# Kernel tuning notes

Hardware: AMD Instinct MI355X
Metric: run time of the kernel (lower is better)

The kernel has to match this reference:

```python
import jax, jax.numpy as jnp
import numpy as np

N, E, G = 50000, 600000, 512   # nodes, edges, graphs
F, D, L = 128, 128, 3          # in_features, hidden dim, num_gc_layers
ED = D * L                      # embedding_dim (readout='concat')
C = 1.0                         # curvature
MIN_NORM = 1e-15
BALL_EPS = 4e-3                 # hgcn PoincareBall proj eps for float32


def _logmap0(p, c):
    sc = jnp.sqrt(c)
    n = jnp.clip(jnp.linalg.norm(p, axis=-1, keepdims=True), MIN_NORM, None)
    return p / (sc * n) * jnp.arctanh(jnp.clip(sc * n, -1 + 1e-15, 1 - 1e-15))


def _expmap0(u, c):
    sc = jnp.sqrt(c)
    n = jnp.clip(jnp.linalg.norm(u, axis=-1, keepdims=True), MIN_NORM, None)
    return jnp.tanh(sc * n) * u / (sc * n)


def _proj(x, c):
    n = jnp.clip(jnp.linalg.norm(x, axis=-1, keepdims=True), MIN_NORM, None)
    maxn = (1.0 - BALL_EPS) / jnp.sqrt(c)
    return jnp.where(n > maxn, x / n * maxn, x)


def _gcn(x, W, b, src, dst):
    h = x @ W
    deg = jax.ops.segment_sum(jnp.ones_like(dst, dtype=h.dtype), dst, num_segments=N) + 1.0
    dinv = deg ** -0.5
    msg = h[src] * (dinv[src] * dinv[dst])[:, None]           # [E, D]
    agg = jax.ops.segment_sum(msg, dst, num_segments=N) + h * (dinv * dinv)[:, None]
    return agg + b


def _encoder(x, Ws, bs, src, dst, batch):
    xs = []
    for W, b in zip(Ws, bs):
        x = jax.nn.relu(_gcn(x, W, b, src, dst))
        xs.append(x)
    # readout='concat' with global_add_pool
    g = jnp.concatenate([jax.ops.segment_sum(h, batch, num_segments=G) for h in xs], axis=1)
    return g, jnp.concatenate(xs, axis=1)


def _mlp(x, W1, W2):  # proj_head: Linear (no bias), ReLU, Linear (no bias)
    return jax.nn.relu(x @ W1) @ W2


def setup_inputs() -> dict:
    key = jax.random.key(0)
    ks = jax.random.split(key, 24)

    def xav(k, i, o):
        return jax.random.normal(k, (i, o), dtype=jnp.float32) * np.float32(np.sqrt(2.0 / (i + o)))

    inp = {
        'x':   jax.random.normal(ks[0], (N, F), dtype=jnp.float32) * 1e-3,  # points inside the ball
        'x_s': jax.random.normal(ks[1], (N, F), dtype=jnp.float32) * 1e-3,
        'src': jax.random.randint(ks[2], (E,), 0, N, dtype=jnp.int32),
        'dst': jax.random.randint(ks[3], (E,), 0, N, dtype=jnp.int32),
        'batch': jnp.sort(jax.random.randint(ks[4], (N,), 0, G, dtype=jnp.int32)),
        # feature-branch GCN encoder
        'Wf0': xav(ks[5], F, D), 'Wf1': xav(ks[6], D, D), 'Wf2': xav(ks[7], D, D),
        'bf0': jnp.zeros((D,), jnp.float32), 'bf1': jnp.zeros((D,), jnp.float32), 'bf2': jnp.zeros((D,), jnp.float32),
        # structure-branch GCN encoder
        'Ws0': xav(ks[8], F, D), 'Ws1': xav(ks[9], D, D), 'Ws2': xav(ks[10], D, D),
        'bs0': jnp.zeros((D,), jnp.float32), 'bs1': jnp.zeros((D,), jnp.float32), 'bs2': jnp.zeros((D,), jnp.float32),
        # proj heads (biases removed by init_emb)
        'P1': xav(ks[11], ED, ED), 'P2': xav(ks[12], ED, ED),
        'G1': xav(ks[13], 2 * ED, ED), 'G2': xav(ks[14], ED, ED),
    }
    return inp


def reference(x, x_s, Wf0, Wf1, Wf2, bf0, bf1, bf2, Ws0, Ws1, Ws2, bs0, bs1, bs2, P1, P2, G1, G2, src, dst, batch):
    xt_f = _logmap0(x, C)
    xt_s = _logmap0(x_s, C)
    g_f, n_f = _encoder(xt_f, (Wf0, Wf1, Wf2), (bf0, bf1, bf2), src, dst, batch)
    g_s, n_s = _encoder(xt_s, (Ws0, Ws1, Ws2), (bs0, bs1, bs2), src, dst, batch)
    g = _mlp(jnp.concatenate((g_f, g_s), axis=1), G1, G2)
    e = lambda t: _proj(_expmap0(t, C), C)
    return (e(g), e(_mlp(g_f, P1, P2)), e(_mlp(n_f, P1, P2)), e(_mlp(g_s, P1, P2)), e(_mlp(n_s, P1, P2)))
```

## Files before the change

### kernel.cpp

```cpp
#include <hip/hip_runtime.h>
#include <math.h>

#define N_NODES 50000
#define N_EDGES 600000
#define N_GRAPHS 512
#define F_IN 128
#define D_HID 128
#define EDIM 384
#define M_ALL (N_NODES + N_GRAPHS)

typedef __attribute__((ext_vector_type(8))) short bf16x8;
typedef __attribute__((ext_vector_type(4))) float f32x4;
typedef __attribute__((ext_vector_type(16))) float f32x16;

static __device__ __forceinline__ float wave_reduce_sum(float s) {
#pragma unroll
  for (int off = 32; off > 0; off >>= 1) s += __shfl_xor(s, off, 64);
  return s;
}

static __device__ __forceinline__ int wave_reduce_sum_i(int s) {
#pragma unroll
  for (int off = 32; off > 0; off >>= 1) s += __shfl_xor(s, off, 64);
  return s;
}

static __device__ __forceinline__ short f2b(float f) {
  unsigned u = __float_as_uint(f);
  unsigned r = (u + 0x7FFFu + ((u >> 16) & 1u)) >> 16;
  return (short)r;
}

static __device__ __forceinline__ float b2f(short s) {
  return __uint_as_float(((unsigned)(unsigned short)s) << 16);
}


#define SCAN_BS 256
#define SCAN_NB ((N_NODES + SCAN_BS - 1) / SCAN_BS)

__global__ __launch_bounds__(SCAN_BS) void init_kernel(const int* __restrict__ batch,
                                                       int* __restrict__ cnt,
                                                       int* __restrict__ gptr) {
  int i = blockIdx.x * SCAN_BS + threadIdx.x;
  if (i < N_NODES) cnt[i] = 0;
  if (i <= N_GRAPHS) {
    int lo = 0, hi = N_NODES;
    while (lo < hi) { int mid = (lo + hi) >> 1; if (batch[mid] < i) lo = mid + 1; else hi = mid; }
    gptr[i] = lo;
  }
}

__global__ void hist_kernel(const int* __restrict__ dst, int* __restrict__ cnt) {
  int i = blockIdx.x * blockDim.x + threadIdx.x;
  if (i < N_EDGES) atomicAdd(&cnt[dst[i]], 1);
}

__global__ __launch_bounds__(SCAN_BS) void scan1_kernel(const int* __restrict__ cnt,
                                                        int* __restrict__ row_ptr,
                                                        int* __restrict__ bsum) {
  __shared__ int wsum[4];
  int tid = threadIdx.x, lane = tid & 63, wid = tid >> 6;
  int idx = blockIdx.x * SCAN_BS + tid;
  int v = (idx < N_NODES) ? cnt[idx] : 0;
  int x = v;
#pragma unroll
  for (int off = 1; off < 64; off <<= 1) {
    int t = __shfl_up(x, off, 64);
    if (lane >= off) x += t;
  }
  if (lane == 63) wsum[wid] = x;
  __syncthreads();
  int pre = 0, tot = 0;
#pragma unroll
  for (int w = 0; w < 4; ++w) { int s = wsum[w]; tot += s; if (w < wid) pre += s; }
  if (idx < N_NODES) row_ptr[idx + 1] = x + pre;
  if (tid == 0) bsum[blockIdx.x] = tot;
}

__global__ __launch_bounds__(SCAN_BS) void scan3_kernel(const int* __restrict__ cnt,
                                                        const int* __restrict__ bsum,
                                                        int* __restrict__ row_ptr,
                                                        int* __restrict__ cursor,
                                                        float* __restrict__ dinv) {
  __shared__ int ws[4];
  int tid = threadIdx.x, lane = tid & 63, wid = tid >> 6;
  int v = 0;
  if (tid < SCAN_NB && tid < blockIdx.x) v = bsum[tid];
  v = wave_reduce_sum_i(v);
  if (lane == 0) ws[wid] = v;
  __syncthreads();
  int boff = ws[0] + ws[1] + ws[2] + ws[3];
  int idx = blockIdx.x * SCAN_BS + tid;
  if (idx >= N_NODES) return;
  int val = row_ptr[idx + 1] + boff;
  row_ptr[idx + 1] = val;
  int c = cnt[idx];
  cursor[idx] = val - c;
  dinv[idx] = 1.0f / sqrtf((float)(c + 1));
  if (idx == 0) row_ptr[0] = 0;
}

__global__ void scatter_kernel(const int* __restrict__ src, const int* __restrict__ dst,
                               const float* __restrict__ dinv, int* __restrict__ cursor,
                               int* __restrict__ col, float* __restrict__ ew) {
  int e = blockIdx.x * blockDim.x + threadIdx.x;
  if (e >= N_EDGES) return;
  int s = src[e], d = dst[e];
  int pos = atomicAdd(&cursor[d], 1);
  col[pos] = s;
  ew[pos] = dinv[s] * dinv[d];
}


struct WcSeg { const float* W; short* Wt; int K; int Nc; };
struct WcArgs { WcSeg seg[10]; };

__global__ void wconv_all_kernel(WcArgs a) {
  int sidx = blockIdx.y;
  WcSeg s = a.seg[sidx];
  int i = blockIdx.x * blockDim.x + threadIdx.x;
  if (i >= s.K * s.Nc) return;
  int k = i / s.Nc, n = i - k * s.Nc;
  s.Wt[(size_t)n * s.K + k] = f2b(s.W[i]);
}


__global__ __launch_bounds__(256) void logmap2_kernel(const float* __restrict__ x,
                                                      const float* __restrict__ x_s,
                                                      short* __restrict__ Ab) {
  int w = blockIdx.x * 4 + (threadIdx.x >> 6);
  int lane = threadIdx.x & 63;
  if (w >= 2 * N_NODES) return;
  int br = (w >= N_NODES) ? 1 : 0;
  int row = br ? (w - N_NODES) : w;
  const float* xr = (br ? x_s : x) + (size_t)row * F_IN;
  float2 v = *(const float2*)(xr + lane * 2);
  float s = wave_reduce_sum(v.x * v.x + v.y * v.y);
  float n = sqrtf(s);
  float nc = fmaxf(n, 1e-15f);
  float f = atanhf(fminf(nc, 0.9999999f)) / nc;
  short2 o; o.x = f2b(v.x * f); o.y = f2b(v.y * f);
  *(short2*)(Ab + (size_t)row * 256 + br * 128 + lane * 2) = o;
}


__global__ __launch_bounds__(256) void agg2_kernel(const short* __restrict__ Xin, int lda,
                                                   const float* __restrict__ dinv,
                                                   const int* __restrict__ row_ptr,
                                                   const int* __restrict__ col,
                                                   const float* __restrict__ ew,
                                                   short* __restrict__ Xa) {
  int node = blockIdx.x * 4 + (threadIdx.x >> 6);
  int lane = threadIdx.x & 63;
  if (node >= N_NODES) return;
  float di = dinv[node];
  float wsf = di * di;
  short4 sv = *(const short4*)(Xin + (size_t)node * lda + lane * 4);
  float a0 = b2f(sv.x) * wsf, a1 = b2f(sv.y) * wsf, a2 = b2f(sv.z) * wsf, a3 = b2f(sv.w) * wsf;
  int s = row_ptr[node], e = row_ptr[node + 1];
  int j = s;
  for (; j + 4 <= e; j += 4) {
    int c0 = col[j], c1 = col[j + 1], c2 = col[j + 2], c3 = col[j + 3];
    float w0 = ew[j], w1 = ew[j + 1], w2 = ew[j + 2], w3 = ew[j + 3];
    short4 v0 = *(const short4*)(Xin + (size_t)c0 * lda + lane * 4);
    short4 v1 = *(const short4*)(Xin + (size_t)c1 * lda + lane * 4);
    short4 v2 = *(const short4*)(Xin + (size_t)c2 * lda + lane * 4);
    short4 v3 = *(const short4*)(Xin + (size_t)c3 * lda + lane * 4);
    a0 += b2f(v0.x) * w0; a1 += b2f(v0.y) * w0; a2 += b2f(v0.z) * w0; a3 += b2f(v0.w) * w0;
    a0 += b2f(v1.x) * w1; a1 += b2f(v1.y) * w1; a2 += b2f(v1.z) * w1; a3 += b2f(v1.w) * w1;
    a0 += b2f(v2.x) * w2; a1 += b2f(v2.y) * w2; a2 += b2f(v2.z) * w2; a3 += b2f(v2.w) * w2;
    a0 += b2f(v3.x) * w3; a1 += b2f(v3.y) * w3; a2 += b2f(v3.z) * w3; a3 += b2f(v3.w) * w3;
  }
  for (; j < e; ++j) {
    float w0 = ew[j];
    short4 v0 = *(const short4*)(Xin + (size_t)col[j] * lda + lane * 4);
    a0 += b2f(v0.x) * w0; a1 += b2f(v0.y) * w0; a2 += b2f(v0.z) * w0; a3 += b2f(v0.w) * w0;
  }
  short4 o; o.x = f2b(a0); o.y = f2b(a1); o.z = f2b(a2); o.w = f2b(a3);
  *(short4*)(Xa + (size_t)node * 256 + lane * 4) = o;
}


#define LDK 40

struct GemmZArgs {
  const short* A[2];
  const short* Bt[2];
  const float* bias[2];
  short* Cb[2];
  int lda, ldc, M, Nc, K, kexp, do_relu;
};

__global__ __launch_bounds__(256) void mfma_gemmz_kernel(GemmZArgs g) {
  __shared__ __align__(16) short As[128 * LDK];
  __shared__ __align__(16) short Bs[128 * LDK];
  int z = blockIdx.z;
  const short* __restrict__ A = g.A[z];
  const short* __restrict__ Bt = g.Bt[z];
  int tid = threadIdx.x;
  int wave = tid >> 6, lane = tid & 63;
  int wr = (wave >> 1) * 64, wc = (wave & 1) * 64;
  int q = lane >> 4, m = lane & 15;
  int row0 = blockIdx.x * 128, col0 = blockIdx.y * 128;
  f32x4 acc[4][4] = {};
  for (int k0 = 0; k0 < g.K; k0 += 32) {
#pragma unroll
    for (int p = 0; p < 2; ++p) {
      int idx = p * 256 + tid;
      int r = idx >> 2, kc = (idx & 3) * 8;
      int gr = row0 + r;
      int kk = k0 + kc;
      int acol = g.kexp ? (kk + ((kk >> 7) << 7)) : kk;
      float4 v = make_float4(0.f, 0.f, 0.f, 0.f);
      if (gr < g.M) v = *(const float4*)(A + (size_t)gr * g.lda + acol);
      *(float4*)(As + r * LDK + kc) = v;
      float4 w = *(const float4*)(Bt + (size_t)(col0 + r) * g.K + kk);
      *(float4*)(Bs + r * LDK + kc) = w;
    }
    __syncthreads();
    bf16x8 af[4], bfr[4];
#pragma unroll
    for (int i = 0; i < 4; ++i) {
      af[i]  = *(const bf16x8*)(As + (wr + i * 16 + m) * LDK + q * 8);
      bfr[i] = *(const bf16x8*)(Bs + (wc + i * 16 + m) * LDK + q * 8);
    }
#pragma unroll
    for (int i = 0; i < 4; ++i)
#pragma unroll
      for (int j = 0; j < 4; ++j)
        acc[i][j] = __builtin_amdgcn_mfma_f32_16x16x32_bf16(af[i], bfr[j], acc[i][j], 0, 0, 0);
    __syncthreads();
  }
  const float* __restrict__ bias = g.bias[z];
  short* __restrict__ Cb = g.Cb[z];
#pragma unroll
  for (int i = 0; i < 4; ++i) {
#pragma unroll
    for (int r = 0; r < 4; ++r) {
      int rr = row0 + wr + i * 16 + q * 4 + r;
      if (rr >= g.M) continue;
#pragma unroll
      for (int j = 0; j < 4; ++j) {
        int cc = col0 + wc + j * 16 + m;
        float v = acc[i][j][r];
        if (bias) v += bias[cc];
        if (g.do_relu) v = fmaxf(v, 0.0f);
        Cb[(size_t)rr * g.ldc + cc] = f2b(v);
      }
    }
  }
}


#define HLD 392

struct MlpProb {
  const short* A;
  const short* B1;
  const short* B2;
  float* Cf;
  float* Cf2;
  int lda, M, K1, kexp, split;
};
struct Mlp2Args { MlpProb p[3]; int gx_h; };

__global__ __launch_bounds__(512) void mlp2_kernel(Mlp2Args g) {
  __shared__ __align__(16) short H[128 * HLD];
  __shared__ float nsum[128][4];
  int z = blockIdx.z;
  int bx = blockIdx.x;
  MlpProb p;
  int row0;
  if (bx < g.gx_h) { p = g.p[z]; row0 = bx * 128; }
  else { if (z) return; p = g.p[2]; row0 = (bx - g.gx_h) * 128; }

  int tid = threadIdx.x;
  int wave = tid >> 6, lane = tid & 63;
  int l31 = lane & 31, lh = lane >> 5;
  int rg = wave & 1;
  int cq = wave >> 1;

  const short* Arow0 = p.A + (size_t)(row0 + rg * 64 + l31) * p.lda;
  const short* Arow1 = Arow0 + (size_t)32 * p.lda;
  const short* B1c0 = p.B1 + (size_t)(cq * 96 + l31) * p.K1;
  const short* B1c1 = B1c0 + (size_t)32 * p.K1;
  const short* B1c2 = B1c1 + (size_t)32 * p.K1;

  f32x16 acc0[2][3] = {};
#pragma unroll 2
  for (int k0 = 0; k0 < p.K1; k0 += 16) {
    int kk = k0 + lh * 8;
    int acol = p.kexp ? (kk + ((kk >> 7) << 7)) : kk;
    bf16x8 a0 = *(const bf16x8*)(Arow0 + acol);
    bf16x8 a1 = *(const bf16x8*)(Arow1 + acol);
    bf16x8 b0 = *(const bf16x8*)(B1c0 + kk);
    bf16x8 b1 = *(const bf16x8*)(B1c1 + kk);
    bf16x8 b2 = *(const bf16x8*)(B1c2 + kk);
    acc0[0][0] = __builtin_amdgcn_mfma_f32_32x32x16_bf16(a0, b0, acc0[0][0], 0, 0, 0);
    acc0[1][0] = __builtin_amdgcn_mfma_f32_32x32x16_bf16(a1, b0, acc0[1][0], 0, 0, 0);
    acc0[0][1] = __builtin_amdgcn_mfma_f32_32x32x16_bf16(a0, b1, acc0[0][1], 0, 0, 0);
    acc0[1][1] = __builtin_amdgcn_mfma_f32_32x32x16_bf16(a1, b1, acc0[1][1], 0, 0, 0);
    acc0[0][2] = __builtin_amdgcn_mfma_f32_32x32x16_bf16(a0, b2, acc0[0][2], 0, 0, 0);
    acc0[1][2] = __builtin_amdgcn_mfma_f32_32x32x16_bf16(a1, b2, acc0[1][2], 0, 0, 0);
  }
#pragma unroll
  for (int rf = 0; rf < 2; ++rf)
#pragma unroll
    for (int f = 0; f < 3; ++f)
#pragma unroll
      for (int reg = 0; reg < 16; ++reg) {
        int rl = rg * 64 + rf * 32 + (reg & 3) + 8 * (reg >> 2) + 4 * lh;
        H[rl * HLD + cq * 96 + f * 32 + l31] = f2b(fmaxf(acc0[rf][f][reg], 0.0f));
      }
  __syncthreads();
  const short* B2c0 = p.B2 + (size_t)(cq * 96 + l31) * 384;
  const short* B2c1 = B2c0 + (size_t)32 * 384;
  const short* B2c2 = B2c1 + (size_t)32 * 384;
  const short* H0 = H + (rg * 64 + l31) * HLD;
  const short* H1 = H0 + 32 * HLD;
  f32x16 acc[2][3] = {};
#pragma unroll 2
  for (int k0 = 0; k0 < 384; k0 += 16) {
    int kk = k0 + lh * 8;
    bf16x8 a0 = *(const bf16x8*)(H0 + kk);
    bf16x8 a1 = *(const bf16x8*)(H1 + kk);
    bf16x8 b0 = *(const bf16x8*)(B2c0 + kk);
    bf16x8 b1 = *(const bf16x8*)(B2c1 + kk);
    bf16x8 b2 = *(const bf16x8*)(B2c2 + kk);
    acc[0][0] = __builtin_amdgcn_mfma_f32_32x32x16_bf16(a0, b0, acc[0][0], 0, 0, 0);
    acc[1][0] = __builtin_amdgcn_mfma_f32_32x32x16_bf16(a1, b0, acc[1][0], 0, 0, 0);
    acc[0][1] = __builtin_amdgcn_mfma_f32_32x32x16_bf16(a0, b1, acc[0][1], 0, 0, 0);
    acc[1][1] = __builtin_amdgcn_mfma_f32_32x32x16_bf16(a1, b1, acc[1][1], 0, 0, 0);
    acc[0][2] = __builtin_amdgcn_mfma_f32_32x32x16_bf16(a0, b2, acc[0][2], 0, 0, 0);
    acc[1][2] = __builtin_amdgcn_mfma_f32_32x32x16_bf16(a1, b2, acc[1][2], 0, 0, 0);
  }
#pragma unroll
  for (int rf = 0; rf < 2; ++rf)
#pragma unroll
    for (int reg = 0; reg < 16; ++reg) {
      float s = acc[rf][0][reg] * acc[rf][0][reg] + acc[rf][1][reg] * acc[rf][1][reg] +
                acc[rf][2][reg] * acc[rf][2][reg];
      s += __shfl_xor(s, 1, 64);
      s += __shfl_xor(s, 2, 64);
      s += __shfl_xor(s, 4, 64);
      s += __shfl_xor(s, 8, 64);
      s += __shfl_xor(s, 16, 64);
      if (l31 == 0)
        nsum[rg * 64 + rf * 32 + (reg & 3) + 8 * (reg >> 2) + 4 * lh][cq] = s;
    }
  __syncthreads();
  const float maxn = 1.0f - 4e-3f;
#pragma unroll
  for (int rf = 0; rf < 2; ++rf)
#pragma unroll
    for (int reg = 0; reg < 16; ++reg) {
      int rl = rg * 64 + rf * 32 + (reg & 3) + 8 * (reg >> 2) + 4 * lh;
      int rr = row0 + rl;
      if (rr >= p.M) continue;
      float s = nsum[rl][0] + nsum[rl][1] + nsum[rl][2] + nsum[rl][3];
      float n = fmaxf(sqrtf(s), 1e-15f);
      float th = tanhf(n);
      float fct = th / n;
      float n2 = fmaxf(th, 1e-15f);
      if (n2 > maxn) fct *= maxn / n2;
      float* base = (rr < p.split) ? (p.Cf + (size_t)rr * 384)
                                   : (p.Cf2 + (size_t)(rr - p.split) * 384);
#pragma unroll
      for (int f = 0; f < 3; ++f)
        base[cq * 96 + f * 32 + l31] = acc[rf][f][reg] * fct;
    }
}


__global__ __launch_bounds__(768) void pool2_kernel(const short* __restrict__ NB,
                                                    const int* __restrict__ gptr,
                                                    short* __restrict__ GCb,
                                                    short* __restrict__ nbappend) {
  int g = blockIdx.x, t = threadIdx.x;
  int s = gptr[g], e = gptr[g + 1];
  float acc = 0.0f;
  for (int i = s; i < e; ++i) acc += b2f(NB[(size_t)i * 768 + t]);
  short bv = f2b(acc);
  int l = t >> 8, rem = t & 255, b = rem >> 7, c = rem & 127;
  GCb[(size_t)g * 768 + b * 384 + l * 128 + c] = bv;
  nbappend[(size_t)g * 768 + t] = bv;
}


extern "C" void kernel_launch(void* const* d_in, const int* in_sizes, int n_in,
                              void* d_out, int out_size, void* d_ws, size_t ws_size,
                              hipStream_t stream) {
  (void)in_sizes; (void)n_in; (void)out_size; (void)ws_size;
  const float* x   = (const float*)d_in[0];
  const float* x_s = (const float*)d_in[1];
  const int* src   = (const int*)d_in[2];
  const int* dst   = (const int*)d_in[3];
  const int* batch = (const int*)d_in[4];
  const float* Wf[3] = {(const float*)d_in[5], (const float*)d_in[6], (const float*)d_in[7]};
  const float* bf[3] = {(const float*)d_in[8], (const float*)d_in[9], (const float*)d_in[10]};
  const float* Wsb[3] = {(const float*)d_in[11], (const float*)d_in[12], (const float*)d_in[13]};
  const float* bs[3] = {(const float*)d_in[14], (const float*)d_in[15], (const float*)d_in[16]};
  const float* P1 = (const float*)d_in[17];
  const float* P2 = (const float*)d_in[18];
  const float* G1 = (const float*)d_in[19];
  const float* G2 = (const float*)d_in[20];
  float* out = (float*)d_out;

  char* w = (char*)d_ws;
  auto alloc = [&](size_t bytes) {
    char* p = w;
    w += (bytes + 255) & ~(size_t)255;
    return p;
  };
  short* Ab    = (short*)alloc((size_t)N_NODES * 256 * 2);
  short* Xa    = (short*)alloc((size_t)N_NODES * 256 * 2);
  short* NB    = (short*)alloc((size_t)M_ALL * 768 * 2);
  int* cnt     = (int*)alloc((size_t)N_NODES * 4);
  int* row_ptr = (int*)alloc((size_t)(N_NODES + 1) * 4);
  int* cursor  = (int*)alloc((size_t)N_NODES * 4);
  float* dinv  = (float*)alloc((size_t)N_NODES * 4);
  int* col     = (int*)alloc((size_t)N_EDGES * 4);
  float* ew    = (float*)alloc((size_t)N_EDGES * 4);
  int* gptr    = (int*)alloc((size_t)(N_GRAPHS + 1) * 4);
  int* bsum    = (int*)alloc(256 * 4);
  short* GCb   = (short*)alloc((size_t)N_GRAPHS * 768 * 2);
  short* P1t   = (short*)alloc((size_t)EDIM * EDIM * 2);
  short* P2t   = (short*)alloc((size_t)EDIM * EDIM * 2);
  short* G1t   = (short*)alloc((size_t)768 * EDIM * 2);
  short* G2t   = (short*)alloc((size_t)EDIM * EDIM * 2);
  short* Wft[3], *Wst[3];
  for (int l = 0; l < 3; ++l) {
    Wft[l] = (short*)alloc((size_t)128 * 128 * 2);
    Wst[l] = (short*)alloc((size_t)128 * 128 * 2);
  }

  {
    WcArgs wa;
    wa.seg[0] = {P1, P1t, EDIM, EDIM};
    wa.seg[1] = {P2, P2t, EDIM, EDIM};
    wa.seg[2] = {G1, G1t, 768, EDIM};
    wa.seg[3] = {G2, G2t, EDIM, EDIM};
    for (int l = 0; l < 3; ++l) {
      wa.seg[4 + l] = {Wf[l], Wft[l], 128, 128};
      wa.seg[7 + l] = {Wsb[l], Wst[l], 128, 128};
    }
    wconv_all_kernel<<<dim3((768 * EDIM + 255) / 256, 10), 256, 0, stream>>>(wa);
  }

  init_kernel<<<SCAN_NB, SCAN_BS, 0, stream>>>(batch, cnt, gptr);
  hist_kernel<<<(N_EDGES + 255) / 256, 256, 0, stream>>>(dst, cnt);
  scan1_kernel<<<SCAN_NB, SCAN_BS, 0, stream>>>(cnt, row_ptr, bsum);
  scan3_kernel<<<SCAN_NB, SCAN_BS, 0, stream>>>(cnt, bsum, row_ptr, cursor, dinv);
  scatter_kernel<<<(N_EDGES + 255) / 256, 256, 0, stream>>>(src, dst, dinv, cursor, col, ew);

  const size_t OUT0 = 0;
  const size_t OUT1 = (size_t)N_GRAPHS * EDIM;
  const size_t OUT2 = OUT1 + (size_t)N_GRAPHS * EDIM;
  const size_t OUT3 = OUT2 + (size_t)N_NODES * EDIM;

  const int gx_layer = (N_NODES + 127) / 128;
  const int gx_mfma  = (M_ALL + 127) / 128;
  const int gx_agg   = (N_NODES + 3) / 4;

  logmap2_kernel<<<(2 * N_NODES + 3) / 4, 256, 0, stream>>>(x, x_s, Ab);

  const short* cur = Ab;
  int clda = 256;
  for (int l = 0; l < 3; ++l) {
    agg2_kernel<<<gx_agg, 256, 0, stream>>>(cur, clda, dinv, row_ptr, col, ew, Xa);
    GemmZArgs ga = {};
    ga.A[0] = Xa;        ga.A[1] = Xa + 128;
    ga.Bt[0] = Wft[l];   ga.Bt[1] = Wst[l];
    ga.bias[0] = bf[l];  ga.bias[1] = bs[l];
    ga.Cb[0] = NB + l * 256;        ga.Cb[1] = NB + l * 256 + 128;
    ga.lda = 256; ga.ldc = 768; ga.M = N_NODES; ga.Nc = 128; ga.K = 128;
    ga.kexp = 0; ga.do_relu = 1;
    mfma_gemmz_kernel<<<dim3(gx_layer, 1, 2), 256, 0, stream>>>(ga);
    cur = NB + l * 256;
    clda = 768;
  }

  pool2_kernel<<<N_GRAPHS, 768, 0, stream>>>(NB, gptr, GCb, NB + (size_t)N_NODES * 768);

  {
    const int gx_g = (N_GRAPHS + 127) / 128;
    Mlp2Args h = {};
    h.p[0] = {NB,       P1t, P2t, out + OUT2,
              out + OUT1, 768, M_ALL, EDIM, 1, N_NODES};
    h.p[1] = {NB + 128, P1t, P2t, out + OUT3 + (size_t)N_GRAPHS * EDIM,
              out + OUT3, 768, M_ALL, EDIM, 1, N_NODES};
    h.p[2] = {GCb, G1t, G2t, out + OUT0, out + OUT0, 768, N_GRAPHS, 768, 0, 1 << 30};
    h.gx_h = gx_mfma;
    mlp2_kernel<<<dim3(gx_mfma + gx_g, 1, 2), 512, 0, stream>>>(h);
  }
}
```

Measured before the change: 835.6 us.

## Stage MLP A and B operand tiles through shared memory in mlp2_kernel

Replaces direct per-wave global loads of A and weight operands in both MLP GEMM stages with cooperative 32-wide K tiles staged in LDS, shared by all eight waves in the block. This is meant to cut redundant global and L2 traffic, since each weight row was previously loaded separately by both row-group waves. It adds two barriers per K step, extra LDS (about 33 KB more) that may lower occupancy, and no double buffering, so load latency is no longer overlapped. It also adds bounds masking on A rows.

```diff
diff --git a/kernel.cpp b/kernel.cpp
--- a/kernel.cpp
+++ b/kernel.cpp
@@ -266,6 +266,8 @@
 struct Mlp2Args { MlpProb p[3]; int gx_h; };
 
 __global__ __launch_bounds__(512) void mlp2_kernel(Mlp2Args g) {
+  __shared__ __align__(16) short As[128 * LDK];
+  __shared__ __align__(16) short Bs[384 * LDK];
   __shared__ __align__(16) short H[128 * HLD];
   __shared__ float nsum[128][4];
   int z = blockIdx.z;
@@ -281,28 +283,41 @@
   int rg = wave & 1;
   int cq = wave >> 1;
 
-  const short* Arow0 = p.A + (size_t)(row0 + rg * 64 + l31) * p.lda;
-  const short* Arow1 = Arow0 + (size_t)32 * p.lda;
-  const short* B1c0 = p.B1 + (size_t)(cq * 96 + l31) * p.K1;
-  const short* B1c1 = B1c0 + (size_t)32 * p.K1;
-  const short* B1c2 = B1c1 + (size_t)32 * p.K1;
-
-  f32x16 acc0[2][3] = {};
-#pragma unroll 2
-  for (int k0 = 0; k0 < p.K1; k0 += 16) {
-    int kk = k0 + lh * 8;
-    int acol = p.kexp ? (kk + ((kk >> 7) << 7)) : kk;
-    bf16x8 a0 = *(const bf16x8*)(Arow0 + acol);
-    bf16x8 a1 = *(const bf16x8*)(Arow1 + acol);
-    bf16x8 b0 = *(const bf16x8*)(B1c0 + kk);
-    bf16x8 b1 = *(const bf16x8*)(B1c1 + kk);
-    bf16x8 b2 = *(const bf16x8*)(B1c2 + kk);
-    acc0[0][0] = __builtin_amdgcn_mfma_f32_32x32x16_bf16(a0, b0, acc0[0][0], 0, 0, 0);
-    acc0[1][0] = __builtin_amdgcn_mfma_f32_32x32x16_bf16(a1, b0, acc0[1][0], 0, 0, 0);
-    acc0[0][1] = __builtin_amdgcn_mfma_f32_32x32x16_bf16(a0, b1, acc0[0][1], 0, 0, 0);
-    acc0[1][1] = __builtin_amdgcn_mfma_f32_32x32x16_bf16(a1, b1, acc0[1][1], 0, 0, 0);
-    acc0[0][2] = __builtin_amdgcn_mfma_f32_32x32x16_bf16(a0, b2, acc0[0][2], 0, 0, 0);
-    acc0[1][2] = __builtin_amdgcn_mfma_f32_32x32x16_bf16(a1, b2, acc0[1][2], 0, 0, 0);
+  f32x16 acc[2][3] = {};
+  for (int k0 = 0; k0 < p.K1; k0 += 32) {
+    {
+      int r = tid >> 2, kc = (tid & 3) * 8;
+      int gr = row0 + r;
+      int kk = k0 + kc;
+      int acol = p.kexp ? (kk + ((kk >> 7) << 7)) : kk;
+      float4 v = make_float4(0.f, 0.f, 0.f, 0.f);
+      if (gr < p.M) v = *(const float4*)(p.A + (size_t)gr * p.lda + acol);
+      *(float4*)(As + r * LDK + kc) = v;
+    }
+#pragma unroll
+    for (int q = 0; q < 3; ++q) {
+      int idx = q * 512 + tid;
+      int r = idx >> 2, kc = (idx & 3) * 8;
+      float4 w0 = *(const float4*)(p.B1 + (size_t)r * p.K1 + k0 + kc);
+      *(float4*)(Bs + r * LDK + kc) = w0;
+    }
+    __syncthreads();
+#pragma unroll
+    for (int ks = 0; ks < 32; ks += 16) {
+      int kloc = ks + lh * 8;
+      bf16x8 a0 = *(const bf16x8*)(As + (rg * 64 + l31) * LDK + kloc);
+      bf16x8 a1 = *(const bf16x8*)(As + (rg * 64 + 32 + l31) * LDK + kloc);
+      bf16x8 b0 = *(const bf16x8*)(Bs + (cq * 96 + l31) * LDK + kloc);
+      bf16x8 b1 = *(const bf16x8*)(Bs + (cq * 96 + 32 + l31) * LDK + kloc);
+      bf16x8 b2 = *(const bf16x8*)(Bs + (cq * 96 + 64 + l31) * LDK + kloc);
+      acc[0][0] = __builtin_amdgcn_mfma_f32_32x32x16_bf16(a0, b0, acc[0][0], 0, 0, 0);
+      acc[1][0] = __builtin_amdgcn_mfma_f32_32x32x16_bf16(a1, b0, acc[1][0], 0, 0, 0);
+      acc[0][1] = __builtin_amdgcn_mfma_f32_32x32x16_bf16(a0, b1, acc[0][1], 0, 0, 0);
+      acc[1][1] = __builtin_amdgcn_mfma_f32_32x32x16_bf16(a1, b1, acc[1][1], 0, 0, 0);
+      acc[0][2] = __builtin_amdgcn_mfma_f32_32x32x16_bf16(a0, b2, acc[0][2], 0, 0, 0);
+      acc[1][2] = __builtin_amdgcn_mfma_f32_32x32x16_bf16(a1, b2, acc[1][2], 0, 0, 0);
+    }
+    __syncthreads();
   }
 #pragma unroll
   for (int rf = 0; rf < 2; ++rf)
@@ -311,29 +326,38 @@
 #pragma unroll
       for (int reg = 0; reg < 16; ++reg) {
         int rl = rg * 64 + rf * 32 + (reg & 3) + 8 * (reg >> 2) + 4 * lh;
-        H[rl * HLD + cq * 96 + f * 32 + l31] = f2b(fmaxf(acc0[rf][f][reg], 0.0f));
+        H[rl * HLD + cq * 96 + f * 32 + l31] = f2b(fmaxf(acc[rf][f][reg], 0.0f));
       }
+#pragma unroll
+  for (int rf = 0; rf < 2; ++rf)
+#pragma unroll
+    for (int f = 0; f < 3; ++f) acc[rf][f] = (f32x16){};
   __syncthreads();
-  const short* B2c0 = p.B2 + (size_t)(cq * 96 + l31) * 384;
-  const short* B2c1 = B2c0 + (size_t)32 * 384;
-  const short* B2c2 = B2c1 + (size_t)32 * 384;
-  const short* H0 = H + (rg * 64 + l31) * HLD;
-  const short* H1 = H0 + 32 * HLD;
-  f32x16 acc[2][3] = {};
-#pragma unroll 2
-  for (int k0 = 0; k0 < 384; k0 += 16) {
-    int kk = k0 + lh * 8;
-    bf16x8 a0 = *(const bf16x8*)(H0 + kk);
-    bf16x8 a1 = *(const bf16x8*)(H1 + kk);
-    bf16x8 b0 = *(const bf16x8*)(B2c0 + kk);
-    bf16x8 b1 = *(const bf16x8*)(B2c1 + kk);
-    bf16x8 b2 = *(const bf16x8*)(B2c2 + kk);
-    acc[0][0] = __builtin_amdgcn_mfma_f32_32x32x16_bf16(a0, b0, acc[0][0], 0, 0, 0);
-    acc[1][0] = __builtin_amdgcn_mfma_f32_32x32x16_bf16(a1, b0, acc[1][0], 0, 0, 0);
-    acc[0][1] = __builtin_amdgcn_mfma_f32_32x32x16_bf16(a0, b1, acc[0][1], 0, 0, 0);
-    acc[1][1] = __builtin_amdgcn_mfma_f32_32x32x16_bf16(a1, b1, acc[1][1], 0, 0, 0);
-    acc[0][2] = __builtin_amdgcn_mfma_f32_32x32x16_bf16(a0, b2, acc[0][2], 0, 0, 0);
-    acc[1][2] = __builtin_amdgcn_mfma_f32_32x32x16_bf16(a1, b2, acc[1][2], 0, 0, 0);
+  for (int k0 = 0; k0 < 384; k0 += 32) {
+#pragma unroll
+    for (int q = 0; q < 3; ++q) {
+      int idx = q * 512 + tid;
+      int r = idx >> 2, kc = (idx & 3) * 8;
+      float4 w0 = *(const float4*)(p.B2 + (size_t)r * 384 + k0 + kc);
+      *(float4*)(Bs + r * LDK + kc) = w0;
+    }
+    __syncthreads();
+#pragma unroll
+    for (int ks = 0; ks < 32; ks += 16) {
+      int kloc = ks + lh * 8;
+      bf16x8 a0 = *(const bf16x8*)(H + (rg * 64 + l31) * HLD + k0 + kloc);
+      bf16x8 a1 = *(const bf16x8*)(H + (rg * 64 + 32 + l31) * HLD + k0 + kloc);
+      bf16x8 b0 = *(const bf16x8*)(Bs + (cq * 96 + l31) * LDK + kloc);
+      bf16x8 b1 = *(const bf16x8*)(Bs + (cq * 96 + 32 + l31) * LDK + kloc);
+      bf16x8 b2 = *(const bf16x8*)(Bs + (cq * 96 + 64 + l31) * LDK + kloc);
+      acc[0][0] = __builtin_amdgcn_mfma_f32_32x32x16_bf16(a0, b0, acc[0][0], 0, 0, 0);
+      acc[1][0] = __builtin_amdgcn_mfma_f32_32x32x16_bf16(a1, b0, acc[1][0], 0, 0, 0);
+      acc[0][1] = __builtin_amdgcn_mfma_f32_32x32x16_bf16(a0, b1, acc[0][1], 0, 0, 0);
+      acc[1][1] = __builtin_amdgcn_mfma_f32_32x32x16_bf16(a1, b1, acc[1][1], 0, 0, 0);
+      acc[0][2] = __builtin_amdgcn_mfma_f32_32x32x16_bf16(a0, b2, acc[0][2], 0, 0, 0);
+      acc[1][2] = __builtin_amdgcn_mfma_f32_32x32x16_bf16(a1, b2, acc[1][2], 0, 0, 0);
+    }
+    __syncthreads();
   }
 #pragma unroll
   for (int rf = 0; rf < 2; ++rf)
```

Result: faster. 748.7 us (-10.4%).
